# Kernel optimization log

Hardware: AMD Instinct MI355X
Metric: run time of the kernel (lower is better)

Reference implementation:

```python
import jax, jax.numpy as jnp
import numpy as np

E, H, M = 1024, 16, 256
B, S = 2, 2048
D = E // H
SCALE = D ** -0.5


def setup_inputs() -> dict:
    key = jax.random.key(0)
    ks = jax.random.split(key, 10)
    p = 0.02
    return {
        "x": jax.random.normal(ks[0], (B, S, E), jnp.float32),
        "Wq": jax.random.normal(ks[1], (E, E), jnp.float32) * p,
        "bq": jax.random.normal(ks[2], (E,), jnp.float32) * p,
        "Wk": jax.random.normal(ks[3], (E, E), jnp.float32) * p,
        "bk": jax.random.normal(ks[4], (E,), jnp.float32) * p,
        "Wv": jax.random.normal(ks[5], (E, E), jnp.float32) * p,
        "bv": jax.random.normal(ks[6], (E,), jnp.float32) * p,
        "Wo": jax.random.normal(ks[7], (E, E), jnp.float32) * p,
        "bo": jax.random.normal(ks[8], (E,), jnp.float32) * p,
        "memory_state": jax.random.normal(ks[9], (M, E), jnp.float32) * p,
    }


def reference(x, Wq, bq, Wk, bk, Wv, bv, Wo, bo, memory_state):
    b, s, e = x.shape
    # QKV projections (torch Linear: y = x W^T + b), split heads -> [b,h,s,d]
    q = (x @ Wq.T + bq).reshape(b, s, H, D).transpose(0, 2, 1, 3)
    k = (x @ Wk.T + bk).reshape(b, s, H, D).transpose(0, 2, 1, 3)
    v = (x @ Wv.T + bv).reshape(b, s, H, D).transpose(0, 2, 1, 3)
    # full self-attention (eval mode: dropout is identity)
    attn = jax.nn.softmax(jnp.einsum("bhqd,bhkd->bhqk", q, k) * SCALE, axis=-1)
    attn_out = jnp.einsum("bhqk,bhkd->bhqd", attn, v)
    attn_out = attn_out.transpose(0, 2, 1, 3).reshape(b, s, e)
    # memory-read cross-attention on raw x against compressed memory [M,E]
    mem_w = jax.nn.softmax(jnp.einsum("bse,me->bsm", x, memory_state) * SCALE, axis=-1)
    mem_out = jnp.einsum("bsm,me->bse", mem_w, memory_state)
    out = attn_out + 0.5 * mem_out
    return out @ Wo.T + bo
```

## Files before the change

### kernel.cpp

```cpp
#include <hip/hip_runtime.h>
#include <cstdint>
#include <cstddef>


typedef __bf16 bf16;
typedef bf16  bf16x8 __attribute__((ext_vector_type(8)));
typedef bf16  bf16x4 __attribute__((ext_vector_type(4)));
typedef float f32x4  __attribute__((ext_vector_type(4)));

#define B_DIM 2
#define S_DIM 2048
#define E_DIM 1024
#define H_DIM 16
#define D_DIM 64
#define M_DIM 256
#define NROW  (B_DIM * S_DIM)
#define C1 0.18033688011112042f

__device__ __forceinline__ void async_cp16(const bf16* g, bf16* l)
{
    __builtin_amdgcn_global_load_lds(
        (const __attribute__((address_space(1))) void*)g,
        (__attribute__((address_space(3))) void*)l, 16, 0, 0);
}

__global__ void __launch_bounds__(256)
conv_all(const float* __restrict__ x,  const float* __restrict__ Wq,
         const float* __restrict__ Wk, const float* __restrict__ Wv,
         const float* __restrict__ Wo, const float* __restrict__ mem,
         bf16* __restrict__ xb,  bf16* __restrict__ Wqb,
         bf16* __restrict__ Wkb, bf16* __restrict__ Wvb,
         bf16* __restrict__ Wob, bf16* __restrict__ memb,
         bf16* __restrict__ memt)
{
    int t = blockIdx.x * 256 + threadIdx.x;
    const float* src; bf16* dst; int off; bool is_mem = false;
    if      (t <  524288) { src = x;   dst = xb;   off = t; }
    else if (t <  655360) { src = Wq;  dst = Wqb;  off = t - 524288; }
    else if (t <  786432) { src = Wk;  dst = Wkb;  off = t - 655360; }
    else if (t <  917504) { src = Wv;  dst = Wvb;  off = t - 786432; }
    else if (t < 1048576) { src = Wo;  dst = Wob;  off = t - 917504; }
    else                  { src = mem; dst = memb; off = t - 1048576; is_mem = true; }
    const float4* p = (const float4*)src + (size_t)off * 2;
    float4 a = p[0], b = p[1];
    bf16x8 o;
    o[0] = (bf16)a.x; o[1] = (bf16)a.y; o[2] = (bf16)a.z; o[3] = (bf16)a.w;
    o[4] = (bf16)b.x; o[5] = (bf16)b.y; o[6] = (bf16)b.z; o[7] = (bf16)b.w;
    *(bf16x8*)(dst + (size_t)off * 8) = o;
    if (is_mem) {
        int r = off >> 7, c0 = (off & 127) * 8;
        float h[8] = {a.x, a.y, a.z, a.w, b.x, b.y, b.z, b.w};
#pragma unroll
        for (int j = 0; j < 8; ++j)
            memt[(size_t)(c0 + j) * M_DIM + r] = (bf16)(0.5f * h[j]);
    }
}

struct GemmAcc { f32x4 a[4][4]; };

__device__ __forceinline__ void
gemm_core(const bf16* __restrict__ A, const bf16* __restrict__ Bm,
          int K, int m0, int n0, bf16* As, bf16* Bs, GemmAcc& R)
{
    const int tid  = threadIdx.x;
    const int lane = tid & 63;
    const int wave = tid >> 6;
    const int quad = lane >> 4;
    const int l16  = lane & 15;
    const int wm   = (wave >> 1) * 64;
    const int wn   = (wave & 1) * 64;

#pragma unroll
    for (int i = 0; i < 4; ++i)
#pragma unroll
        for (int j = 0; j < 4; ++j)
            R.a[i][j] = f32x4{0.f, 0.f, 0.f, 0.f};

    int s_c0  = wave * 128 + lane;
    int s_r0  = s_c0 >> 2;
    int s_k0  = (s_c0 & 3) ^ ((s_r0 >> 1) & 3);
    int s_c1  = s_c0 + 64;
    int s_r1  = s_c1 >> 2;
    int s_k1  = (s_c1 & 3) ^ ((s_r1 >> 1) & 3);
    const bf16* gA0 = A  + (size_t)(m0 + s_r0) * K + s_k0 * 8;
    const bf16* gA1 = A  + (size_t)(m0 + s_r1) * K + s_k1 * 8;
    const bf16* gB0 = Bm + (size_t)(n0 + s_r0) * K + s_k0 * 8;
    const bf16* gB1 = Bm + (size_t)(n0 + s_r1) * K + s_k1 * 8;

#define STAGE(buf, k0)                                                     \
    do {                                                                   \
        async_cp16(gA0 + (k0), &As[(buf) * 4096 + wave * 1024]);           \
        async_cp16(gA1 + (k0), &As[(buf) * 4096 + wave * 1024 + 512]);     \
        async_cp16(gB0 + (k0), &Bs[(buf) * 4096 + wave * 1024]);           \
        async_cp16(gB1 + (k0), &Bs[(buf) * 4096 + wave * 1024 + 512]);     \
    } while (0)

    STAGE(0, 0);
    int buf = 0;
    for (int k0 = 0; k0 < K; k0 += 32) {
        __syncthreads();
        if (k0 + 32 < K) STAGE(buf ^ 1, k0 + 32);

        const bf16* Ab = As + buf * 4096;
        const bf16* Bb = Bs + buf * 4096;
        bf16x8 af[4], bfr[4];
#pragma unroll
        for (int mi = 0; mi < 4; ++mi) {
            int m    = wm + mi * 16 + l16;
            int slot = quad ^ ((m >> 1) & 3);
            af[mi]   = *(const bf16x8*)(&Ab[(m * 4 + slot) * 8]);
        }
#pragma unroll
        for (int ni = 0; ni < 4; ++ni) {
            int n    = wn + ni * 16 + l16;
            int slot = quad ^ ((n >> 1) & 3);
            bfr[ni]  = *(const bf16x8*)(&Bb[(n * 4 + slot) * 8]);
        }
#pragma unroll
        for (int mi = 0; mi < 4; ++mi)
#pragma unroll
            for (int ni = 0; ni < 4; ++ni)
                R.a[mi][ni] = __builtin_amdgcn_mfma_f32_16x16x32_bf16(
                    af[mi], bfr[ni], R.a[mi][ni], 0, 0, 0);
        buf ^= 1;
    }
#undef STAGE
}

template <typename OUT_T>
__global__ void __launch_bounds__(256, 3)
gemm_nt(const bf16* __restrict__ A, const bf16* __restrict__ Bm,
        const float* __restrict__ bias, OUT_T* __restrict__ C,
        int N, int K)
{
    __shared__ __align__(16) bf16 As[2 * 4096];
    __shared__ __align__(16) bf16 Bs[2 * 4096];
    const int m0 = blockIdx.y * 128, n0 = blockIdx.x * 128;
    GemmAcc R;
    gemm_core(A, Bm, K, m0, n0, As, Bs, R);
    const int lane = threadIdx.x & 63, wave = threadIdx.x >> 6;
    const int quad = lane >> 4, l16 = lane & 15;
    const int wm = (wave >> 1) * 64, wn = (wave & 1) * 64;
#pragma unroll
    for (int ni = 0; ni < 4; ++ni) {
        int col  = n0 + wn + ni * 16 + l16;
        float bv = bias ? bias[col] : 0.f;
#pragma unroll
        for (int mi = 0; mi < 4; ++mi)
#pragma unroll
            for (int r = 0; r < 4; ++r) {
                int rowg = m0 + wm + mi * 16 + quad * 4 + r;
                C[(size_t)rowg * N + col] = (OUT_T)(R.a[mi][ni][r] + bv);
            }
    }
}

__global__ void __launch_bounds__(256, 3)
gemm_qkvl(const bf16* __restrict__ A,
          const bf16* __restrict__ Wq, const bf16* __restrict__ Wk,
          const bf16* __restrict__ Wv, const bf16* __restrict__ memb,
          const float* __restrict__ bq, const float* __restrict__ bk,
          const float* __restrict__ bv,
          bf16* __restrict__ q, bf16* __restrict__ k,
          bf16* __restrict__ vt, bf16* __restrict__ lg)
{
    __shared__ __align__(16) bf16 As[2 * 4096];
    __shared__ __align__(16) bf16 Bs[2 * 4096];
    const int x    = blockIdx.x;
    const int widx = (x < 24) ? (x >> 3) : 3;
    const int n0   = (x < 24) ? (x & 7) * 128 : (x - 24) * 128;
    const int m0   = blockIdx.y * 128;
    const bf16*  Bm = (widx == 0) ? Wq : (widx == 1) ? Wk :
                      (widx == 2) ? Wv : memb;
    GemmAcc R;
    gemm_core(A, Bm, E_DIM, m0, n0, As, Bs, R);

    const int lane = threadIdx.x & 63, wave = threadIdx.x >> 6;
    const int quad = lane >> 4, l16 = lane & 15;
    const int wm = (wave >> 1) * 64, wn = (wave & 1) * 64;

    if (widx == 0 || widx == 1) {
        bf16* C = (widx == 0) ? q : k;
        const float* bi = (widx == 0) ? bq : bk;
        float scale = (widx == 0) ? C1 : 1.0f;
#pragma unroll
        for (int ni = 0; ni < 4; ++ni) {
            int col  = n0 + wn + ni * 16 + l16;
            float bb = bi[col];
#pragma unroll
            for (int mi = 0; mi < 4; ++mi)
#pragma unroll
                for (int r = 0; r < 4; ++r) {
                    int rowg = m0 + wm + mi * 16 + quad * 4 + r;
                    C[(size_t)rowg * E_DIM + col] =
                        (bf16)((R.a[mi][ni][r] + bb) * scale);
                }
        }
    } else if (widx == 2) {
#pragma unroll
        for (int ni = 0; ni < 4; ++ni) {
            int col = n0 + wn + ni * 16 + l16;
            float bb = bv[col];
#pragma unroll
            for (int mi = 0; mi < 4; ++mi) {
                int row0 = m0 + wm + mi * 16 + quad * 4;
                int bidx = row0 >> 11, s = row0 & 2047;
                bf16x4 pk;
#pragma unroll
                for (int r = 0; r < 4; ++r) pk[r] = (bf16)(R.a[mi][ni][r] + bb);
                *(bf16x4*)(&vt[((size_t)(bidx * H_DIM) * 64 + col) * S_DIM + s]) = pk;
            }
        }
    } else {
#pragma unroll
        for (int ni = 0; ni < 4; ++ni) {
            int col = n0 + wn + ni * 16 + l16;
#pragma unroll
            for (int mi = 0; mi < 4; ++mi)
#pragma unroll
                for (int r = 0; r < 4; ++r) {
                    int rowg = m0 + wm + mi * 16 + quad * 4 + r;
                    lg[(size_t)rowg * M_DIM + col] = (bf16)R.a[mi][ni][r];
                }
        }
    }
}

__global__ void __launch_bounds__(256)
softmax_mem(bf16* __restrict__ P)
{
    const int tid  = threadIdx.x;
    const int lane = tid & 63;
    const int wave = tid >> 6;
    const int row  = blockIdx.x * 4 + wave;
    bf16* lp = P + (size_t)row * M_DIM;

    bf16x4 raw = *(const bf16x4*)(lp + lane * 4);
    float t[4];
#pragma unroll
    for (int j = 0; j < 4; ++j) t[j] = (float)raw[j] * C1;

    float m = fmaxf(fmaxf(t[0], t[1]), fmaxf(t[2], t[3]));
#pragma unroll
    for (int s = 1; s < 64; s <<= 1) m = fmaxf(m, __shfl_xor(m, s));

    float p[4], sum = 0.f;
#pragma unroll
    for (int j = 0; j < 4; ++j) { p[j] = exp2f(t[j] - m); sum += p[j]; }
#pragma unroll
    for (int s = 1; s < 64; s <<= 1) sum += __shfl_xor(sum, s);

    float inv = 1.f / sum;
    bf16x4 o;
#pragma unroll
    for (int j = 0; j < 4; ++j) o[j] = (bf16)(p[j] * inv);
    *(bf16x4*)(lp + lane * 4) = o;
}

__global__ void __launch_bounds__(256, 2)
flash_attn(const bf16* __restrict__ q, const bf16* __restrict__ k,
           const bf16* __restrict__ vt, const bf16* __restrict__ Pmem,
           const bf16* __restrict__ memt, bf16* __restrict__ outc)
{
    __shared__ __align__(16) bf16 Ks[2 * 4096];
    __shared__ __align__(16) bf16 Vs[2 * 4096];
    const int tid  = threadIdx.x;
    const int lane = tid & 63;
    const int wave = tid >> 6;
    const int quad = lane >> 4;
    const int l16  = lane & 15;
    const int lid = blockIdx.x;
    const int xcd = lid & 7;
    const int kk  = lid >> 3;
    const int qt  = kk & 15;
    const int p   = ((kk >> 4) << 3) | xcd;
    const int b   = p >> 4;
    const int h   = p & 15;
    const int q0  = qt * 128 + wave * 32;

    const bf16* qb = q  + (size_t)(b * S_DIM + q0) * E_DIM + h * D_DIM;
    const bf16* kb = k  + (size_t)(b * S_DIM) * E_DIM + h * D_DIM;
    const bf16* vb = vt + (size_t)(b * H_DIM + h) * D_DIM * S_DIM;

    const int s_s0 = wave * 128 + lane;
    const int s_r0 = s_s0 >> 3;
    const int s_g0 = (s_s0 & 7) ^ (s_r0 & 7);
    const int s_s1 = s_s0 + 64;
    const int s_r1 = s_s1 >> 3;
    const int s_g1 = (s_s1 & 7) ^ (s_r1 & 7);
    const bf16* gK0 = kb + (size_t)s_r0 * E_DIM + s_g0 * 8;
    const bf16* gK1 = kb + (size_t)s_r1 * E_DIM + s_g1 * 8;
    const bf16* gV0 = vb + (size_t)s_r0 * S_DIM + s_g0 * 8;
    const bf16* gV1 = vb + (size_t)s_r1 * S_DIM + s_g1 * 8;

#define STAGE_KV(buf, kt)                                                   \
    do {                                                                    \
        async_cp16(gK0 + (size_t)(kt) * E_DIM, &Ks[(buf) * 4096 + wave * 1024]);       \
        async_cp16(gK1 + (size_t)(kt) * E_DIM, &Ks[(buf) * 4096 + wave * 1024 + 512]); \
        async_cp16(gV0 + (kt), &Vs[(buf) * 4096 + wave * 1024]);            \
        async_cp16(gV1 + (kt), &Vs[(buf) * 4096 + wave * 1024 + 512]);      \
    } while (0)

    bf16x8 a_q[2][2];
#pragma unroll
    for (int mf = 0; mf < 2; ++mf)
#pragma unroll
        for (int kc = 0; kc < 2; ++kc)
            a_q[mf][kc] = *(const bf16x8*)(
                qb + (size_t)(mf * 16 + l16) * E_DIM + kc * 32 + quad * 8);

    f32x4 o_acc[2][4];
#pragma unroll
    for (int mf = 0; mf < 2; ++mf)
#pragma unroll
        for (int i = 0; i < 4; ++i) o_acc[mf][i] = f32x4{0.f, 0.f, 0.f, 0.f};
    float l_part[2] = {0.f, 0.f};

    STAGE_KV(0, 0);
    int buf = 0;
    for (int kt = 0; kt < S_DIM; kt += 64) {
        __syncthreads();
        if (kt + 64 < S_DIM) STAGE_KV(buf ^ 1, kt + 64);
        const bf16* Kb = Ks + buf * 4096;
        const bf16* Vb = Vs + buf * 4096;

        f32x4 sc[2][4];
#pragma unroll
        for (int nb = 0; nb < 4; ++nb) {
            bf16x8 bk0, bk1;
            {
                int row = nb * 16 + l16;
                int sl0 = quad ^ (row & 7);
                int sl1 = (4 + quad) ^ (row & 7);
                bk0 = *(const bf16x8*)(&Kb[row * 64 + sl0 * 8]);
                bk1 = *(const bf16x8*)(&Kb[row * 64 + sl1 * 8]);
            }
#pragma unroll
            for (int mf = 0; mf < 2; ++mf) {
                f32x4 a = f32x4{0.f, 0.f, 0.f, 0.f};
                a = __builtin_amdgcn_mfma_f32_16x16x32_bf16(bk0, a_q[mf][0], a, 0, 0, 0);
                a = __builtin_amdgcn_mfma_f32_16x16x32_bf16(bk1, a_q[mf][1], a, 0, 0, 0);
                sc[mf][nb] = a;
            }
        }

        bf16x8 bv[4][2];
#pragma unroll
        for (int nd = 0; nd < 4; ++nd)
#pragma unroll
            for (int kc = 0; kc < 2; ++kc) {
                int row  = nd * 16 + l16;
                int slot = (kc * 4 + quad) ^ (row & 7);
                bv[nd][kc] = *(const bf16x8*)(&Vb[row * 64 + slot * 8]);
            }

        asm volatile("s_waitcnt lgkmcnt(0)\n\ts_barrier" ::: "memory");

        bf16* pw = ((wave < 2) ? Ks : Vs) + buf * 4096 + (wave & 1) * 2048;
#pragma unroll
        for (int mf = 0; mf < 2; ++mf)
#pragma unroll
            for (int nb = 0; nb < 4; ++nb) {
                bf16x4 pk;
#pragma unroll
                for (int r = 0; r < 4; ++r) {
                    float e = exp2f(sc[mf][nb][r]);
                    l_part[mf] += e;
                    pk[r] = (bf16)e;
                }
                int slot = (nb * 2 + (quad >> 1)) ^ (l16 & 7);
                *(bf16x4*)(&pw[(mf * 16 + l16) * 64 + slot * 8 + (quad & 1) * 4]) = pk;
            }

        bf16x8 a_p[2][2];
#pragma unroll
        for (int mf = 0; mf < 2; ++mf)
#pragma unroll
            for (int kc = 0; kc < 2; ++kc) {
                int slot = (kc * 4 + quad) ^ (l16 & 7);
                a_p[mf][kc] = *(const bf16x8*)(&pw[(mf * 16 + l16) * 64 + slot * 8]);
            }

#pragma unroll
        for (int nd = 0; nd < 4; ++nd)
#pragma unroll
            for (int mf = 0; mf < 2; ++mf) {
                o_acc[mf][nd] = __builtin_amdgcn_mfma_f32_16x16x32_bf16(
                    a_p[mf][0], bv[nd][0], o_acc[mf][nd], 0, 0, 0);
                o_acc[mf][nd] = __builtin_amdgcn_mfma_f32_16x16x32_bf16(
                    a_p[mf][1], bv[nd][1], o_acc[mf][nd], 0, 0, 0);
            }
        buf ^= 1;
    }
#undef STAGE_KV

    float linv[2][4];
#pragma unroll
    for (int mf = 0; mf < 2; ++mf) {
        float L = l_part[mf];
        L += __shfl_xor(L, 16);
        L += __shfl_xor(L, 32);
        float Li = 1.f / L;
#pragma unroll
        for (int r = 0; r < 4; ++r)
            linv[mf][r] = __shfl(Li, quad * 4 + r);
    }

    f32x4 macc[2][4];
#pragma unroll
    for (int mf = 0; mf < 2; ++mf)
#pragma unroll
        for (int i = 0; i < 4; ++i) macc[mf][i] = f32x4{0.f, 0.f, 0.f, 0.f};
    const bf16* Pr = Pmem + (size_t)(b * S_DIM + q0) * M_DIM;
    const bf16* Mt = memt + (size_t)(h * D_DIM) * M_DIM;
#pragma unroll
    for (int kc = 0; kc < 8; ++kc) {
        bf16x8 ap[2];
#pragma unroll
        for (int mf = 0; mf < 2; ++mf)
            ap[mf] = *(const bf16x8*)(
                Pr + (size_t)(mf * 16 + l16) * M_DIM + kc * 32 + quad * 8);
#pragma unroll
        for (int nd = 0; nd < 4; ++nd) {
            bf16x8 bm = *(const bf16x8*)(
                Mt + (size_t)(nd * 16 + l16) * M_DIM + kc * 32 + quad * 8);
#pragma unroll
            for (int mf = 0; mf < 2; ++mf)
                macc[mf][nd] = __builtin_amdgcn_mfma_f32_16x16x32_bf16(
                    ap[mf], bm, macc[mf][nd], 0, 0, 0);
        }
    }

    bf16* ob = outc + (size_t)(b * S_DIM + q0) * E_DIM + h * D_DIM;
#pragma unroll
    for (int mf = 0; mf < 2; ++mf)
#pragma unroll
        for (int nd = 0; nd < 4; ++nd)
#pragma unroll
            for (int r = 0; r < 4; ++r) {
                size_t off = (size_t)(mf * 16 + quad * 4 + r) * E_DIM + nd * 16 + l16;
                ob[off] = (bf16)(o_acc[mf][nd][r] * linv[mf][r] + macc[mf][nd][r]);
            }
}

extern "C" void kernel_launch(void* const* d_in, const int* in_sizes, int n_in,
                              void* d_out, int out_size, void* d_ws, size_t ws_size,
                              hipStream_t stream)
{
    (void)in_sizes; (void)n_in; (void)out_size; (void)ws_size;
    const float* x   = (const float*)d_in[0];
    const float* Wq  = (const float*)d_in[1];
    const float* bq  = (const float*)d_in[2];
    const float* Wk  = (const float*)d_in[3];
    const float* bk  = (const float*)d_in[4];
    const float* Wv  = (const float*)d_in[5];
    const float* bv  = (const float*)d_in[6];
    const float* Wo  = (const float*)d_in[7];
    const float* bo  = (const float*)d_in[8];
    const float* mem = (const float*)d_in[9];
    float* out = (float*)d_out;

    bf16* w = (bf16*)d_ws;
    const size_t NE = (size_t)NROW * E_DIM;
    const size_t EE = (size_t)E_DIM * E_DIM;
    bf16* xb      = w;
    bf16* q_ws    = w + NE;
    bf16* k_ws    = w + 2 * NE;
    bf16* Wqb     = w + 3 * NE;
    bf16* Wkb     = Wqb + EE;
    bf16* Wvb     = Wkb + EE;
    bf16* Wob     = Wvb + EE;
    bf16* memb    = Wob + EE;
    bf16* lg_ws   = memb + (size_t)M_DIM * E_DIM;
    bf16* memt_ws = lg_ws + (size_t)NROW * M_DIM;
    bf16* vt_ws = (bf16*)d_out;

    dim3 blk(256);

    conv_all<<<dim3(4224), blk, 0, stream>>>(
        x, Wq, Wk, Wv, Wo, mem, xb, Wqb, Wkb, Wvb, Wob, memb, memt_ws);

    gemm_qkvl<<<dim3(26, NROW / 128), blk, 0, stream>>>(
        xb, Wqb, Wkb, Wvb, memb, bq, bk, bv, q_ws, k_ws, vt_ws, lg_ws);

    softmax_mem<<<dim3(NROW / 4), blk, 0, stream>>>(lg_ws);

    flash_attn<<<dim3(512), blk, 0, stream>>>(
        q_ws, k_ws, vt_ws, lg_ws, memt_ws, q_ws);

    gemm_nt<float><<<dim3(E_DIM / 128, NROW / 128), blk, 0, stream>>>(
        q_ws, Wob, bo, out, E_DIM, E_DIM);
}
```

Measured before the change: 247.7 us.

## Fuse memory softmax into attention, shrink attention blocks, use 64-row output GEMM

```diff
diff --git a/kernel.cpp b/kernel.cpp
--- a/kernel.cpp
+++ b/kernel.cpp
@@ -127,34 +127,6 @@
 #undef STAGE
 }
 
-template <typename OUT_T>
-__global__ void __launch_bounds__(256, 3)
-gemm_nt(const bf16* __restrict__ A, const bf16* __restrict__ Bm,
-        const float* __restrict__ bias, OUT_T* __restrict__ C,
-        int N, int K)
-{
-    __shared__ __align__(16) bf16 As[2 * 4096];
-    __shared__ __align__(16) bf16 Bs[2 * 4096];
-    const int m0 = blockIdx.y * 128, n0 = blockIdx.x * 128;
-    GemmAcc R;
-    gemm_core(A, Bm, K, m0, n0, As, Bs, R);
-    const int lane = threadIdx.x & 63, wave = threadIdx.x >> 6;
-    const int quad = lane >> 4, l16 = lane & 15;
-    const int wm = (wave >> 1) * 64, wn = (wave & 1) * 64;
-#pragma unroll
-    for (int ni = 0; ni < 4; ++ni) {
-        int col  = n0 + wn + ni * 16 + l16;
-        float bv = bias ? bias[col] : 0.f;
-#pragma unroll
-        for (int mi = 0; mi < 4; ++mi)
-#pragma unroll
-            for (int r = 0; r < 4; ++r) {
-                int rowg = m0 + wm + mi * 16 + quad * 4 + r;
-                C[(size_t)rowg * N + col] = (OUT_T)(R.a[mi][ni][r] + bv);
-            }
-    }
-}
-
 __global__ void __launch_bounds__(256, 3)
 gemm_qkvl(const bf16* __restrict__ A,
           const bf16* __restrict__ Wq, const bf16* __restrict__ Wk,
@@ -226,40 +198,96 @@
     }
 }
 
-__global__ void __launch_bounds__(256)
-softmax_mem(bf16* __restrict__ P)
-{
+__global__ void __launch_bounds__(256, 2)
+gemm_out64(const bf16* __restrict__ A, const bf16* __restrict__ Bm,
+           const float* __restrict__ bias, float* __restrict__ C)
+{
+    __shared__ __align__(16) bf16 As[2 * 2048];
+    __shared__ __align__(16) bf16 Bs[2 * 4096];
     const int tid  = threadIdx.x;
     const int lane = tid & 63;
     const int wave = tid >> 6;
-    const int row  = blockIdx.x * 4 + wave;
-    bf16* lp = P + (size_t)row * M_DIM;
-
-    bf16x4 raw = *(const bf16x4*)(lp + lane * 4);
-    float t[4];
-#pragma unroll
-    for (int j = 0; j < 4; ++j) t[j] = (float)raw[j] * C1;
-
-    float m = fmaxf(fmaxf(t[0], t[1]), fmaxf(t[2], t[3]));
-#pragma unroll
-    for (int s = 1; s < 64; s <<= 1) m = fmaxf(m, __shfl_xor(m, s));
-
-    float p[4], sum = 0.f;
-#pragma unroll
-    for (int j = 0; j < 4; ++j) { p[j] = exp2f(t[j] - m); sum += p[j]; }
-#pragma unroll
-    for (int s = 1; s < 64; s <<= 1) sum += __shfl_xor(sum, s);
-
-    float inv = 1.f / sum;
-    bf16x4 o;
-#pragma unroll
-    for (int j = 0; j < 4; ++j) o[j] = (bf16)(p[j] * inv);
-    *(bf16x4*)(lp + lane * 4) = o;
-}
-
-__global__ void __launch_bounds__(256, 2)
+    const int quad = lane >> 4;
+    const int l16  = lane & 15;
+    const int wm   = (wave >> 1) * 32;
+    const int wn   = (wave & 1) * 64;
+    const int m0   = blockIdx.y * 64;
+    const int n0   = blockIdx.x * 128;
+    const int K    = E_DIM;
+
+    f32x4 acc[2][4];
+#pragma unroll
+    for (int i = 0; i < 2; ++i)
+#pragma unroll
+        for (int j = 0; j < 4; ++j) acc[i][j] = f32x4{0.f, 0.f, 0.f, 0.f};
+
+    int a_s  = wave * 64 + lane;
+    int a_r  = a_s >> 2;
+    int a_k  = (a_s & 3) ^ ((a_r >> 1) & 3);
+    int b_s0 = wave * 128 + lane;
+    int b_r0 = b_s0 >> 2;
+    int b_k0 = (b_s0 & 3) ^ ((b_r0 >> 1) & 3);
+    int b_s1 = b_s0 + 64;
+    int b_r1 = b_s1 >> 2;
+    int b_k1 = (b_s1 & 3) ^ ((b_r1 >> 1) & 3);
+    const bf16* gA  = A  + (size_t)(m0 + a_r) * K + a_k * 8;
+    const bf16* gB0 = Bm + (size_t)(n0 + b_r0) * K + b_k0 * 8;
+    const bf16* gB1 = Bm + (size_t)(n0 + b_r1) * K + b_k1 * 8;
+
+#define STAGE64(buf, k0)                                                   \
+    do {                                                                   \
+        async_cp16(gA  + (k0), &As[(buf) * 2048 + wave * 512]);            \
+        async_cp16(gB0 + (k0), &Bs[(buf) * 4096 + wave * 1024]);           \
+        async_cp16(gB1 + (k0), &Bs[(buf) * 4096 + wave * 1024 + 512]);     \
+    } while (0)
+
+    STAGE64(0, 0);
+    int buf = 0;
+    for (int k0 = 0; k0 < K; k0 += 32) {
+        __syncthreads();
+        if (k0 + 32 < K) STAGE64(buf ^ 1, k0 + 32);
+        const bf16* Ab = As + buf * 2048;
+        const bf16* Bb = Bs + buf * 4096;
+        bf16x8 af[2], bfr[4];
+#pragma unroll
+        for (int mi = 0; mi < 2; ++mi) {
+            int m    = wm + mi * 16 + l16;
+            int slot = quad ^ ((m >> 1) & 3);
+            af[mi]   = *(const bf16x8*)(&Ab[(m * 4 + slot) * 8]);
+        }
+#pragma unroll
+        for (int ni = 0; ni < 4; ++ni) {
+            int n    = wn + ni * 16 + l16;
+            int slot = quad ^ ((n >> 1) & 3);
+            bfr[ni]  = *(const bf16x8*)(&Bb[(n * 4 + slot) * 8]);
+        }
+#pragma unroll
+        for (int mi = 0; mi < 2; ++mi)
+#pragma unroll
+            for (int ni = 0; ni < 4; ++ni)
+                acc[mi][ni] = __builtin_amdgcn_mfma_f32_16x16x32_bf16(
+                    af[mi], bfr[ni], acc[mi][ni], 0, 0, 0);
+        buf ^= 1;
+    }
+#undef STAGE64
+
+#pragma unroll
+    for (int ni = 0; ni < 4; ++ni) {
+        int col  = n0 + wn + ni * 16 + l16;
+        float bb = bias[col];
+#pragma unroll
+        for (int mi = 0; mi < 2; ++mi)
+#pragma unroll
+            for (int r = 0; r < 4; ++r) {
+                int rowg = m0 + wm + mi * 16 + quad * 4 + r;
+                C[(size_t)rowg * E_DIM + col] = acc[mi][ni][r] + bb;
+            }
+    }
+}
+
+__global__ void __launch_bounds__(128, 2)
 flash_attn(const bf16* __restrict__ q, const bf16* __restrict__ k,
-           const bf16* __restrict__ vt, const bf16* __restrict__ Pmem,
+           const bf16* __restrict__ vt, const bf16* __restrict__ lg,
            const bf16* __restrict__ memt, bf16* __restrict__ outc)
 {
     __shared__ __align__(16) bf16 Ks[2 * 4096];
@@ -272,33 +300,36 @@
     const int lid = blockIdx.x;
     const int xcd = lid & 7;
     const int kk  = lid >> 3;
-    const int qt  = kk & 15;
-    const int p   = ((kk >> 4) << 3) | xcd;
+    const int qt  = kk & 31;
+    const int p   = ((kk >> 5) << 3) | xcd;
     const int b   = p >> 4;
     const int h   = p & 15;
-    const int q0  = qt * 128 + wave * 32;
+    const int q0  = qt * 64 + wave * 32;
 
     const bf16* qb = q  + (size_t)(b * S_DIM + q0) * E_DIM + h * D_DIM;
     const bf16* kb = k  + (size_t)(b * S_DIM) * E_DIM + h * D_DIM;
     const bf16* vb = vt + (size_t)(b * H_DIM + h) * D_DIM * S_DIM;
 
-    const int s_s0 = wave * 128 + lane;
-    const int s_r0 = s_s0 >> 3;
-    const int s_g0 = (s_s0 & 7) ^ (s_r0 & 7);
-    const int s_s1 = s_s0 + 64;
-    const int s_r1 = s_s1 >> 3;
-    const int s_g1 = (s_s1 & 7) ^ (s_r1 & 7);
-    const bf16* gK0 = kb + (size_t)s_r0 * E_DIM + s_g0 * 8;
-    const bf16* gK1 = kb + (size_t)s_r1 * E_DIM + s_g1 * 8;
-    const bf16* gV0 = vb + (size_t)s_r0 * S_DIM + s_g0 * 8;
-    const bf16* gV1 = vb + (size_t)s_r1 * S_DIM + s_g1 * 8;
-
-#define STAGE_KV(buf, kt)                                                   \
-    do {                                                                    \
-        async_cp16(gK0 + (size_t)(kt) * E_DIM, &Ks[(buf) * 4096 + wave * 1024]);       \
-        async_cp16(gK1 + (size_t)(kt) * E_DIM, &Ks[(buf) * 4096 + wave * 1024 + 512]); \
-        async_cp16(gV0 + (kt), &Vs[(buf) * 4096 + wave * 1024]);            \
-        async_cp16(gV1 + (kt), &Vs[(buf) * 4096 + wave * 1024 + 512]);      \
+    const bf16* gK[4];
+    const bf16* gV[4];
+#pragma unroll
+    for (int j = 0; j < 4; ++j) {
+        int s  = (wave * 4 + j) * 64 + lane;
+        int r  = s >> 3;
+        int gc = (s & 7) ^ (r & 7);
+        gK[j] = kb + (size_t)r * E_DIM + gc * 8;
+        gV[j] = vb + (size_t)r * S_DIM + gc * 8;
+    }
+
+#define STAGE_KV(buf, kt)                                                      \
+    do {                                                                       \
+        _Pragma("unroll")                                                      \
+        for (int j = 0; j < 4; ++j) {                                          \
+            async_cp16(gK[j] + (size_t)(kt) * E_DIM,                           \
+                       &Ks[(buf) * 4096 + (wave * 4 + j) * 512]);              \
+            async_cp16(gV[j] + (kt),                                           \
+                       &Vs[(buf) * 4096 + (wave * 4 + j) * 512]);              \
+        }                                                                      \
     } while (0)
 
     bf16x8 a_q[2][2];
@@ -327,14 +358,11 @@
         f32x4 sc[2][4];
 #pragma unroll
         for (int nb = 0; nb < 4; ++nb) {
-            bf16x8 bk0, bk1;
-            {
-                int row = nb * 16 + l16;
-                int sl0 = quad ^ (row & 7);
-                int sl1 = (4 + quad) ^ (row & 7);
-                bk0 = *(const bf16x8*)(&Kb[row * 64 + sl0 * 8]);
-                bk1 = *(const bf16x8*)(&Kb[row * 64 + sl1 * 8]);
-            }
+            int row = nb * 16 + l16;
+            int sl0 = quad ^ (row & 7);
+            int sl1 = (4 + quad) ^ (row & 7);
+            bf16x8 bk0 = *(const bf16x8*)(&Kb[row * 64 + sl0 * 8]);
+            bf16x8 bk1 = *(const bf16x8*)(&Kb[row * 64 + sl1 * 8]);
 #pragma unroll
             for (int mf = 0; mf < 2; ++mf) {
                 f32x4 a = f32x4{0.f, 0.f, 0.f, 0.f};
@@ -344,19 +372,9 @@
             }
         }
 
-        bf16x8 bv[4][2];
-#pragma unroll
-        for (int nd = 0; nd < 4; ++nd)
-#pragma unroll
-            for (int kc = 0; kc < 2; ++kc) {
-                int row  = nd * 16 + l16;
-                int slot = (kc * 4 + quad) ^ (row & 7);
-                bv[nd][kc] = *(const bf16x8*)(&Vb[row * 64 + slot * 8]);
-            }
-
         asm volatile("s_waitcnt lgkmcnt(0)\n\ts_barrier" ::: "memory");
 
-        bf16* pw = ((wave < 2) ? Ks : Vs) + buf * 4096 + (wave & 1) * 2048;
+        bf16* pw = Ks + buf * 4096 + wave * 2048;
 #pragma unroll
         for (int mf = 0; mf < 2; ++mf)
 #pragma unroll
@@ -382,14 +400,20 @@
             }
 
 #pragma unroll
-        for (int nd = 0; nd < 4; ++nd)
+        for (int nd = 0; nd < 4; ++nd) {
+            int row  = nd * 16 + l16;
+            int sl0  = quad ^ (row & 7);
+            int sl1  = (4 + quad) ^ (row & 7);
+            bf16x8 bv0 = *(const bf16x8*)(&Vb[row * 64 + sl0 * 8]);
+            bf16x8 bv1 = *(const bf16x8*)(&Vb[row * 64 + sl1 * 8]);
 #pragma unroll
             for (int mf = 0; mf < 2; ++mf) {
                 o_acc[mf][nd] = __builtin_amdgcn_mfma_f32_16x16x32_bf16(
-                    a_p[mf][0], bv[nd][0], o_acc[mf][nd], 0, 0, 0);
+                    a_p[mf][0], bv0, o_acc[mf][nd], 0, 0, 0);
                 o_acc[mf][nd] = __builtin_amdgcn_mfma_f32_16x16x32_bf16(
-                    a_p[mf][1], bv[nd][1], o_acc[mf][nd], 0, 0, 0);
-            }
+                    a_p[mf][1], bv1, o_acc[mf][nd], 0, 0, 0);
+            }
+        }
         buf ^= 1;
     }
 #undef STAGE_KV
@@ -406,20 +430,41 @@
             linv[mf][r] = __shfl(Li, quad * 4 + r);
     }
 
+    const bf16* Pr = lg   + (size_t)(b * S_DIM + q0) * M_DIM;
+    const bf16* Mt = memt + (size_t)(h * D_DIM) * M_DIM;
+    float msum[2] = {0.f, 0.f};
+    bf16x8 ep[2][8];
+#pragma unroll
+    for (int kc = 0; kc < 8; ++kc)
+#pragma unroll
+        for (int mf = 0; mf < 2; ++mf) {
+            bf16x8 raw = *(const bf16x8*)(
+                Pr + (size_t)(mf * 16 + l16) * M_DIM + kc * 32 + quad * 8);
+#pragma unroll
+            for (int j = 0; j < 8; ++j) {
+                float e = exp2f(C1 * (float)raw[j]);
+                msum[mf] += e;
+                ep[mf][kc][j] = (bf16)e;
+            }
+        }
+    float minv[2][4];
+#pragma unroll
+    for (int mf = 0; mf < 2; ++mf) {
+        float L = msum[mf];
+        L += __shfl_xor(L, 16);
+        L += __shfl_xor(L, 32);
+        float Li = 1.f / L;
+#pragma unroll
+        for (int r = 0; r < 4; ++r)
+            minv[mf][r] = __shfl(Li, quad * 4 + r);
+    }
     f32x4 macc[2][4];
 #pragma unroll
     for (int mf = 0; mf < 2; ++mf)
 #pragma unroll
         for (int i = 0; i < 4; ++i) macc[mf][i] = f32x4{0.f, 0.f, 0.f, 0.f};
-    const bf16* Pr = Pmem + (size_t)(b * S_DIM + q0) * M_DIM;
-    const bf16* Mt = memt + (size_t)(h * D_DIM) * M_DIM;
-#pragma unroll
-    for (int kc = 0; kc < 8; ++kc) {
-        bf16x8 ap[2];
-#pragma unroll
-        for (int mf = 0; mf < 2; ++mf)
-            ap[mf] = *(const bf16x8*)(
-                Pr + (size_t)(mf * 16 + l16) * M_DIM + kc * 32 + quad * 8);
+#pragma unroll
+    for (int kc = 0; kc < 8; ++kc)
 #pragma unroll
         for (int nd = 0; nd < 4; ++nd) {
             bf16x8 bm = *(const bf16x8*)(
@@ -427,9 +472,8 @@
 #pragma unroll
             for (int mf = 0; mf < 2; ++mf)
                 macc[mf][nd] = __builtin_amdgcn_mfma_f32_16x16x32_bf16(
-                    ap[mf], bm, macc[mf][nd], 0, 0, 0);
-        }
-    }
+                    ep[mf][kc], bm, macc[mf][nd], 0, 0, 0);
+        }
 
     bf16* ob = outc + (size_t)(b * S_DIM + q0) * E_DIM + h * D_DIM;
 #pragma unroll
@@ -439,7 +483,8 @@
 #pragma unroll
             for (int r = 0; r < 4; ++r) {
                 size_t off = (size_t)(mf * 16 + quad * 4 + r) * E_DIM + nd * 16 + l16;
-                ob[off] = (bf16)(o_acc[mf][nd][r] * linv[mf][r] + macc[mf][nd][r]);
+                ob[off] = (bf16)(o_acc[mf][nd][r] * linv[mf][r] +
+                                 macc[mf][nd][r] * minv[mf][r]);
             }
 }
 
@@ -468,11 +513,13 @@
     bf16* k_ws    = w + 2 * NE;
     bf16* Wqb     = w + 3 * NE;
     bf16* Wkb     = Wqb + EE;
+    bf16* Wkb2    = Wkb;
     bf16* Wvb     = Wkb + EE;
     bf16* Wob     = Wvb + EE;
     bf16* memb    = Wob + EE;
     bf16* lg_ws   = memb + (size_t)M_DIM * E_DIM;
     bf16* memt_ws = lg_ws + (size_t)NROW * M_DIM;
+    (void)Wkb2;
     bf16* vt_ws = (bf16*)d_out;
 
     dim3 blk(256);
@@ -483,11 +530,9 @@
     gemm_qkvl<<<dim3(26, NROW / 128), blk, 0, stream>>>(
         xb, Wqb, Wkb, Wvb, memb, bq, bk, bv, q_ws, k_ws, vt_ws, lg_ws);
 
-    softmax_mem<<<dim3(NROW / 4), blk, 0, stream>>>(lg_ws);
-
-    flash_attn<<<dim3(512), blk, 0, stream>>>(
+    flash_attn<<<dim3(1024), dim3(128), 0, stream>>>(
         q_ws, k_ws, vt_ws, lg_ws, memt_ws, q_ws);
 
-    gemm_nt<float><<<dim3(E_DIM / 128, NROW / 128), blk, 0, stream>>>(
-        q_ws, Wob, bo, out, E_DIM, E_DIM);
-}
+    gemm_out64<<<dim3(E_DIM / 128, NROW / 64), blk, 0, stream>>>(
+        q_ws, Wob, bo, out);
+}
```

After: 242.7 us. -2.0%, faster.
